# Kernel optimization log

Hardware: AMD Instinct MI355X
Metric: run time of the kernel (lower is better)

Reference implementation:

```python
import jax, jax.numpy as jnp
import numpy as np

N_FFT = 2048
HOP = 512
SR = 48000
T = 2_880_000  # 60 s stereo @ 48 kHz, multiple of HOP


def _hann(n):
    # torch.hann_window default (periodic=True)
    return (0.5 - 0.5 * jnp.cos(2.0 * jnp.pi * jnp.arange(n) / n)).astype(jnp.float32)


def _stft(x, win):
    # x: [C, T] -> [C, F, bins] complex64 (torch.stft center=True, reflect pad)
    pad = N_FFT // 2
    xp = jnp.pad(x, ((0, 0), (pad, pad)), mode='reflect')
    n_frames = 1 + (xp.shape[-1] - N_FFT) // HOP
    idx = jnp.arange(n_frames)[:, None] * HOP + jnp.arange(N_FFT)[None, :]
    frames = xp[:, idx] * win  # [C, F, N_FFT]
    return jnp.fft.rfft(frames, axis=-1)


def _istft(S, win, length):
    # S: [C, F, bins] -> [C, length]; overlap-add with window-square normalization
    frames = jnp.fft.irfft(S, n=N_FFT, axis=-1) * win  # [C, F, N_FFT]
    nF = frames.shape[1]
    total = (nF - 1) * HOP + N_FFT
    idx = jnp.arange(nF)[:, None] * HOP + jnp.arange(N_FFT)[None, :]
    ola = jnp.zeros((frames.shape[0], total), frames.dtype).at[:, idx].add(frames)
    wsum = jnp.zeros((total,), win.dtype).at[idx].add(jnp.broadcast_to(win ** 2, idx.shape))
    out = ola / jnp.where(wsum > 1e-11, wsum, 1.0)
    pad = N_FFT // 2
    return out[:, pad:pad + length]


def _eq_band(audio, freq, gain_db, q=1.0):
    win = _hann(N_FFT)
    S = _stft(audio, win)  # [C, F, bins]
    bins = S.shape[-1]
    freqs = jnp.linspace(0.0, 24000.0, bins)
    mask = jnp.exp(-((freqs - freq) / (freq / q)) ** 2)  # [bins]
    g_lin = 10.0 ** (gain_db / 20.0)
    S = S * (1.0 + (g_lin - 1.0) * mask)
    return _istft(S, win, audio.shape[-1])


def _compress(audio, threshold, ratio, attack, release, makeup_gain):
    aa = jnp.abs(audio) + 1e-8
    adb = 20.0 * jnp.log10(aa)
    gr = jnp.maximum(adb - threshold, 0.0) * (1.0 - 1.0 / ratio)  # [C, T]
    a_att = 1.0 - jnp.exp(-1.0 / (attack * SR))
    a_rel = 1.0 - jnp.exp(-1.0 / (release * SR))

    def step(prev, g):
        alpha = jnp.where(g > prev, a_att, a_rel)
        new = (1.0 - alpha) * prev + alpha * g
        return new, new

    init = jnp.zeros((audio.shape[0],), audio.dtype)
    _, gs = jax.lax.scan(step, init, gr[:, 1:].T)  # [T-1, C]
    gain_smooth = jnp.concatenate([init[:, None], gs.T], axis=1)  # [C, T]
    gain_lin = 10.0 ** ((-gain_smooth + makeup_gain) / 20.0)
    return jnp.sign(audio) * aa * gain_lin


def setup_inputs() -> dict:
    key = jax.random.key(0)
    audio = 0.1 * jax.random.normal(key, (2, T), dtype=jnp.float32)
    f32 = lambda v: jnp.float32(v)
    return {
        'audio': audio,
        'eq_low_gain': f32(3.0),
        'eq_low_mid_gain': f32(-2.0),
        'eq_high_mid_gain': f32(2.5),
        'eq_high_gain': f32(1.5),
        'comp_threshold': f32(-18.0),
        'comp_ratio': f32(4.0),
        'comp_attack': f32(0.01),
        'comp_release': f32(0.1),
        'comp_makeup_gain': f32(3.0),
        'saturation': f32(1.5),
    }


def reference(audio, eq_low_gain, eq_low_mid_gain, eq_high_mid_gain, eq_high_gain,
              comp_threshold, comp_ratio, comp_attack, comp_release,
              comp_makeup_gain, saturation):
    x = _eq_band(audio, 100.0, eq_low_gain)
    x = _eq_band(x, 500.0, eq_low_mid_gain)
    x = _eq_band(x, 3000.0, eq_high_mid_gain)
    x = _eq_band(x, 10000.0, eq_high_gain)
    x = _compress(x, comp_threshold, comp_ratio, comp_attack, comp_release, comp_makeup_gain)
    # saturation branch (original: python if on .item(); here jnp.where)
    return jnp.where(saturation > 1.0, jnp.tanh(x * saturation) / saturation, x)
```

## Files before the change

kernel.cpp:

```cpp
#include <hip/hip_runtime.h>
#include <math.h>

#define T_LEN   2880000
#define LASTFR  5625
#define NBLK_EQ 625
#define SEG     7680
#define NSEG    375
#define KREC    15
#define NREC    512
#define PROWS   528
#define RST     384
#define PL      (PROWS * RST)
#define SPL     (NREC * RST)

typedef float2 c2;
__device__ __forceinline__ c2 cadd(c2 a, c2 b){ return make_float2(a.x+b.x, a.y+b.y); }
__device__ __forceinline__ c2 csub(c2 a, c2 b){ return make_float2(a.x-b.x, a.y-b.y); }
__device__ __forceinline__ c2 cmul(c2 a, c2 b){ return make_float2(a.x*b.x - a.y*b.y, a.x*b.y + a.y*b.x); }
__device__ __forceinline__ c2 cmulj(c2 a, c2 b){ return make_float2(a.x*b.x + a.y*b.y, a.y*b.x - a.x*b.y); }

template<int SGN>
__device__ __forceinline__ void dft8(c2 v[8]) {
    const float r = 0.70710678118654752f;
    c2 t0 = cadd(v[0], v[4]), t1 = csub(v[0], v[4]);
    c2 t2 = cadd(v[2], v[6]), t3 = csub(v[2], v[6]);
    c2 u0 = cadd(v[1], v[5]), u1 = csub(v[1], v[5]);
    c2 u2 = cadd(v[3], v[7]), u3 = csub(v[3], v[7]);
    c2 t3r = (SGN < 0) ? make_float2(t3.y, -t3.x) : make_float2(-t3.y, t3.x);
    c2 u3r = (SGN < 0) ? make_float2(u3.y, -u3.x) : make_float2(-u3.y, u3.x);
    c2 E0 = cadd(t0, t2), E2 = csub(t0, t2);
    c2 E1 = cadd(t1, t3r), E3 = csub(t1, t3r);
    c2 O0 = cadd(u0, u2), O2 = csub(u0, u2);
    c2 O1 = cadd(u1, u3r), O3 = csub(u1, u3r);
    c2 O1w = (SGN < 0) ? make_float2(r*(O1.x+O1.y), r*(O1.y-O1.x))
                       : make_float2(r*(O1.x-O1.y), r*(O1.x+O1.y));
    c2 O2w = (SGN < 0) ? make_float2(O2.y, -O2.x) : make_float2(-O2.y, O2.x);
    c2 O3w = (SGN < 0) ? make_float2(r*(O3.y-O3.x), -r*(O3.x+O3.y))
                       : make_float2(-r*(O3.x+O3.y), r*(O3.x-O3.y));
    v[0] = cadd(E0, O0);  v[4] = csub(E0, O0);
    v[1] = cadd(E1, O1w); v[5] = csub(E1, O1w);
    v[2] = cadd(E2, O2w); v[6] = csub(E2, O2w);
    v[3] = cadd(E3, O3w); v[7] = csub(E3, O3w);
}

__device__ __forceinline__ c2 shx(c2 v, int m) {
    return make_float2(__shfl_xor(v.x, m), __shfl_xor(v.y, m));
}

__device__ __forceinline__ void emit_chunk(float* __restrict__ dst, const float* __restrict__ WN,
                                           int cchunk, int tid, c2 r0, c2 r1) {
    const bool edge = (cchunk <= 2) || (cchunk >= 5626);
    #pragma unroll
    for (int q = 0; q < 2; ++q) {
        c2 rr = (q == 0) ? r0 : r1;
        int m = cchunk * 512 + (q << 8) + tid;
        float inv = 0.66666666666667f;
        if (edge) {
            int tmn = (m >= 2048) ? (((m - 2048) >> 9) + 1) : 0;
            int tmx = min(LASTFR, m >> 9);
            float wsum = 0.0f;
            for (int tt = tmn; tt <= tmx; ++tt) {
                float w = WN[m - (tt << 9)];
                wsum += w * w;
            }
            inv = (wsum > 1e-11f) ? (1.0f / wsum) : 1.0f;
        }
        int o = m - 1024;
        dst[o]         = rr.x * inv;
        dst[T_LEN + o] = rr.y * inv;
    }
}

__global__ __launch_bounds__(256) void eq_band_kernel(
    const float* __restrict__ src, float* __restrict__ dst,
    const float* __restrict__ gain_db_p, const float f0)
{
    __shared__ c2 SA[2048];
    __shared__ c2 TWs1[2048];
    __shared__ c2 TWs2[256];
    __shared__ c2 TWs3[32];
    __shared__ float MKs[2048];
    __shared__ float WN[2048];

    const int tid = threadIdx.x;
    const int b   = blockIdx.x;

    const float gdb   = *gain_db_p;
    const float g_lin = exp2f(gdb * 0.16609640474436813f);
    const float gm1   = g_lin - 1.0f;

    const float st2048 = 6.283185307179586f / 2048.0f;
    for (int idx = tid; idx < 2048; idx += 256) {
        int m = idx >> 8, j = idx & 255;
        float ang = st2048 * (float)(j * m);
        TWs1[idx] = make_float2(cosf(ang), -sinf(ang));
        WN[idx] = 0.5f - 0.5f * cosf(st2048 * (float)idx);
        int tt = idx & 255;
        int bb = tt >> 2, jj = tt & 3;
        int qrev = ((jj & 1) << 1) | (jj >> 1);
        int k = (bb >> 3) + ((bb & 7) << 3) + (m << 6) + (qrev << 9);
        int kk = (k > 1024) ? (2048 - k) : k;
        float f = (float)kk * (24000.0f / 1024.0f);
        float d = (f - f0) / f0;
        MKs[idx] = (1.0f + gm1 * expf(-d * d)) * (1.0f / 2048.0f);
    }
    {
        int m = tid >> 5, j2 = tid & 31;
        float ang = (6.283185307179586f / 256.0f) * (float)(j2 * m);
        TWs2[tid] = make_float2(cosf(ang), -sinf(ang));
    }
    if (tid < 32) {
        int m = tid >> 2, j = tid & 3;
        float ang = (6.283185307179586f / 32.0f) * (float)(j * m);
        TWs3[tid] = make_float2(cosf(ang), -sinf(ang));
    }
    __syncthreads();

    const int t0   = max(0, 9 * b - 1);
    const int t1   = min(LASTFR, 9 * b + 10);
    const int cmin = 9 * b + 2;
    const int cmax = 9 * b + 10;

    c2 ring[8];
    #pragma unroll
    for (int q = 0; q < 8; ++q) ring[q] = make_float2(0.0f, 0.0f);

    for (int t = t0; t <= t1; ++t) {
        for (int j = tid; j < 2048; j += 256) {
            int ss = t * 512 + j - 1024;
            ss = (ss < 0) ? -ss : ss;
            ss = (ss >= T_LEN) ? (2 * T_LEN - 2 - ss) : ss;
            float w = WN[j];
            SA[j] = make_float2(src[ss] * w, src[T_LEN + ss] * w);
        }
        __syncthreads();

        c2 v[8];

        #pragma unroll
        for (int k = 0; k < 8; ++k) v[k] = SA[tid + (k << 8)];
        dft8<-1>(v);
        #pragma unroll
        for (int m = 1; m < 8; ++m) v[m] = cmul(v[m], TWs1[(m << 8) + tid]);
        #pragma unroll
        for (int m = 0; m < 8; ++m) SA[tid + (m << 8)] = v[m];
        __syncthreads();

        {
            int c = tid >> 5, j2 = tid & 31;
            int base = (c << 8) + j2;
            #pragma unroll
            for (int k = 0; k < 8; ++k) v[k] = SA[base + (k << 5)];
            dft8<-1>(v);
            #pragma unroll
            for (int m = 1; m < 8; ++m) v[m] = cmul(v[m], TWs2[(m << 5) + j2]);
            __syncthreads();
            #pragma unroll
            for (int m = 0; m < 8; ++m) SA[(c << 8) + (m << 5) + (j2 ^ (m << 2))] = v[m];
        }
        __syncthreads();

        {
            int bb = tid >> 2, j = tid & 3;
            int base = bb << 5, bx = (bb & 7) << 2;
            #pragma unroll
            for (int k = 0; k < 8; ++k) v[k] = SA[base + ((k << 2) ^ bx) + j];
            dft8<-1>(v);
            #pragma unroll
            for (int m = 1; m < 8; ++m) v[m] = cmul(v[m], TWs3[(m << 2) + j]);
            #pragma unroll
            for (int m = 0; m < 8; ++m) {
                c2 w = v[m];
                c2 p = shx(w, 2);
                c2 e  = (j & 2) ? csub(p, w) : cadd(w, p);
                c2 qq = shx(e, 1);
                c2 lo = (j & 1) ? csub(qq, e) : cadd(e, qq);
                c2 hi = (j & 1) ? make_float2(qq.x - e.y, qq.y + e.x)
                                : make_float2(e.x + qq.y, e.y - qq.x);
                w = (j & 2) ? hi : lo;
                float mk = MKs[(m << 8) + tid];
                w.x *= mk; w.y *= mk;
                c2 p2 = shx(w, 1);
                c2 e2 = (j & 1) ? csub(p2, w) : cadd(w, p2);
                c2 q2 = shx(e2, 2);
                c2 lo2 = (j & 1) ? make_float2(e2.x - q2.y, e2.y + q2.x)
                                 : cadd(e2, q2);
                c2 hi2 = (j & 1) ? make_float2(q2.x + e2.y, q2.y - e2.x)
                                 : csub(q2, e2);
                v[m] = (j & 2) ? hi2 : lo2;
            }
            #pragma unroll
            for (int m = 1; m < 8; ++m) v[m] = cmulj(v[m], TWs3[(m << 2) + j]);
            dft8<+1>(v);
            __syncthreads();
            #pragma unroll
            for (int k = 0; k < 8; ++k) SA[base + ((k << 2) ^ bx) + j] = v[k];
        }
        __syncthreads();

        {
            int c = tid >> 5, j2 = tid & 31;
            #pragma unroll
            for (int m = 0; m < 8; ++m) v[m] = SA[(c << 8) + (m << 5) + (j2 ^ (m << 2))];
            #pragma unroll
            for (int m = 1; m < 8; ++m) v[m] = cmulj(v[m], TWs2[(m << 5) + j2]);
            dft8<+1>(v);
            __syncthreads();
            #pragma unroll
            for (int k = 0; k < 8; ++k) SA[(c << 8) + (k << 5) + j2] = v[k];
        }
        __syncthreads();

        {
            #pragma unroll
            for (int m = 0; m < 8; ++m) v[m] = SA[tid + (m << 8)];
            #pragma unroll
            for (int m = 1; m < 8; ++m) v[m] = cmulj(v[m], TWs1[(m << 8) + tid]);
            dft8<+1>(v);
            #pragma unroll
            for (int k = 0; k < 8; ++k) {
                float w = WN[tid + (k << 8)];
                ring[k].x += v[k].x * w;
                ring[k].y += v[k].y * w;
            }
        }
        __syncthreads();

        if (t >= cmin) emit_chunk(dst, WN, t, tid, ring[0], ring[1]);
        #pragma unroll
        for (int q = 0; q < 6; ++q) ring[q] = ring[q + 2];
        ring[6] = make_float2(0.0f, 0.0f);
        ring[7] = make_float2(0.0f, 0.0f);
    }
    for (int c = t1 + 1; c <= cmax; ++c) {
        emit_chunk(dst, WN, c, tid, ring[0], ring[1]);
        #pragma unroll
        for (int q = 0; q < 6; ++q) ring[q] = ring[q + 2];
        ring[6] = make_float2(0.0f, 0.0f);
        ring[7] = make_float2(0.0f, 0.0f);
    }
}

__device__ __forceinline__ float gaval(float v, float thr, float coef) {
    float aa = fabsf(v) + 1e-8f;
    return fmaxf(6.020599913279624f * __log2f(aa) - thr, 0.0f) * coef;
}

__global__ __launch_bounds__(256) void rec15_kernel(
    const float* __restrict__ y, float4* __restrict__ rec,
    const float* __restrict__ thr_p, const float* __restrict__ ratio_p,
    const float* __restrict__ att_p, const float* __restrict__ rel_p)
{
    __shared__ float4 Lsub[32][9][4];
    const int r0 = blockIdx.x * 32;
    const int s0 = blockIdx.y * 64;
    const int c  = blockIdx.z;
    const int tid = threadIdx.x;

    float thr = *thr_p, ratio = *ratio_p;
    float A  = expf(-1.0f / ((*att_p) * 48000.0f));
    float Bc = expf(-1.0f / ((*rel_p) * 48000.0f));
    float ra = (1.0f - Bc) / (1.0f - A);
    float coef = (1.0f - 1.0f / ratio) * (1.0f - A);

    const int rr = tid & 31, cg = tid >> 5;
    const int orow = tid >> 3, oc8 = tid & 7;

    #pragma unroll 1
    for (int it = 0; it < 8; ++it) {
        int s = s0 + it * 8 + cg;
        if (s < NSEG) {
            int r = r0 + rr;
            int li = s * SEG + KREC * r;
            const float* yp = y + (long)c * T_LEN + li;
            float I[16];
            float a = gaval(yp[0], thr, coef);
            if (li == 0) a = 0.0f;
            I[0] = a; I[1] = ra * a;
            #pragma unroll
            for (int n = 1; n < KREC; ++n) {
                a = gaval(yp[n], thr, coef);
                float b = ra * a;
                I[n + 1] = fmaf(Bc, I[n], b);
                #pragma unroll
                for (int j = n; j >= 1; --j)
                    I[j] = fmaxf(fmaf(A, I[j], a), fmaf(Bc, I[j - 1], b));
                I[0] = fmaf(A, I[0], a);
            }
            Lsub[rr][cg][0] = make_float4(I[0],  I[1],  I[2],  I[3]);
            Lsub[rr][cg][1] = make_float4(I[4],  I[5],  I[6],  I[7]);
            Lsub[rr][cg][2] = make_float4(I[8],  I[9],  I[10], I[11]);
            Lsub[rr][cg][3] = make_float4(I[12], I[13], I[14], I[15]);
        }
        __syncthreads();
        int so = s0 + it * 8 + oc8;
        if (so < NSEG) {
            #pragma unroll
            for (int q = 0; q < 4; ++q)
                rec[(long)(c * 4 + q) * PL + (r0 + orow) * RST + 4 + so]
                    = Lsub[orow][oc8][q];
        }
        __syncthreads();
    }
}


struct Rec { float4 a, b, c, d; };

__device__ __forceinline__ void load8(Rec (&bb)[8],
    const float4* p0, const float4* p1, const float4* p2, const float4* p3, int r)
{
    #pragma unroll
    for (int k = 0; k < 8; ++k) {
        int o = (r + k) * RST;
        bb[k].a = p0[o]; bb[k].b = p1[o]; bb[k].c = p2[o]; bb[k].d = p3[o];
    }
}

template<bool STORE>
__device__ __forceinline__ void consume8(Rec (&bb)[8], float* sp, int r, float& p,
                                         const float (&S)[16])
{
    #pragma unroll
    for (int k = 0; k < 8; ++k) {
        Rec v = bb[k];
        float m0 = fmaxf(fmaf(S[0],  p, v.a.x), fmaf(S[1],  p, v.a.y));
        float m1 = fmaxf(fmaf(S[2],  p, v.a.z), fmaf(S[3],  p, v.a.w));
        float m2 = fmaxf(fmaf(S[4],  p, v.b.x), fmaf(S[5],  p, v.b.y));
        float m3 = fmaxf(fmaf(S[6],  p, v.b.z), fmaf(S[7],  p, v.b.w));
        float m4 = fmaxf(fmaf(S[8],  p, v.c.x), fmaf(S[9],  p, v.c.y));
        float m5 = fmaxf(fmaf(S[10], p, v.c.z), fmaf(S[11], p, v.c.w));
        float m6 = fmaxf(fmaf(S[12], p, v.d.x), fmaf(S[13], p, v.d.y));
        float m7 = fmaxf(fmaf(S[14], p, v.d.z), fmaf(S[15], p, v.d.w));
        m0 = fmaxf(m0, m1); m2 = fmaxf(m2, m3);
        m4 = fmaxf(m4, m5); m6 = fmaxf(m6, m7);
        m0 = fmaxf(m0, m2); m4 = fmaxf(m4, m6);
        p = fmaxf(m0, m4);
        if (STORE) sp[(r + k) * RST] = p;
    }
}

template<bool STORE>
__device__ void scan_pass(const float4* p0, const float4* p1, const float4* p2,
                          const float4* p3, float* sp, float& p, const float (&S)[16])
{
    Rec bA[8], bB[8];
    load8(bA, p0, p1, p2, p3, 0);
    __builtin_amdgcn_sched_barrier(0);
    int r = 0;
    #pragma unroll 1
    for (int gg = 0; gg < NREC / 16; ++gg) {
        load8(bB, p0, p1, p2, p3, r + 8);
        __builtin_amdgcn_sched_barrier(0);
        consume8<STORE>(bA, sp, r, p, S);
        __builtin_amdgcn_sched_barrier(0);
        load8(bA, p0, p1, p2, p3, r + 16);
        __builtin_amdgcn_sched_barrier(0);
        consume8<STORE>(bB, sp, r + 8, p, S);
        __builtin_amdgcn_sched_barrier(0);
        r += 16;
    }
}

template<int MODE>
__global__ __launch_bounds__(64, 1) void scan_iter_kernel(
    const float4* __restrict__ rec, float* __restrict__ gsP,
    const float* __restrict__ eIn, float* __restrict__ eOut,
    const float* __restrict__ att_p, const float* __restrict__ rel_p)
{
    int gid = blockIdx.x * 64 + threadIdx.x;
    int g2 = min(gid, 2 * NSEG - 1);
    int c = g2 / NSEG;
    int s = g2 - c * NSEG;

    float A  = expf(-1.0f / ((*att_p) * 48000.0f));
    float Bc = expf(-1.0f / ((*rel_p) * 48000.0f));
    float S[16];
    {
        float pa = 1.0f;
        #pragma unroll
        for (int j = 15; j >= 0; --j) { S[j] = pa; pa *= A; }
        float pb = 1.0f;
        #pragma unroll
        for (int j = 0; j < 16; ++j) { S[j] *= pb; pb *= Bc; }
    }

    float p = 0.0f;
    if (MODE != 0) p = (s == 0) ? 0.0f : eIn[c * NSEG + s - 1];

    const float4* p0 = rec + (long)(c * 4 + 0) * PL + 4 + s;
    const float4* p1 = rec + (long)(c * 4 + 1) * PL + 4 + s;
    const float4* p2 = rec + (long)(c * 4 + 2) * PL + 4 + s;
    const float4* p3 = rec + (long)(c * 4 + 3) * PL + 4 + s;

    if (MODE == 2) {
        float* sbase = gsP + (long)c * SPL + 4 + s;
        scan_pass<true>(p0, p1, p2, p3, sbase, p, S);
    } else {
        scan_pass<false>(p0, p1, p2, p3, nullptr, p, S);
        eOut[c * NSEG + s] = p;
    }
}

__global__ __launch_bounds__(256) void final_kernel(
    const float* __restrict__ y, const float* __restrict__ gsP, float* __restrict__ out,
    const float* __restrict__ thr_p, const float* __restrict__ ratio_p,
    const float* __restrict__ att_p, const float* __restrict__ rel_p,
    const float* __restrict__ mk_p, const float* __restrict__ sat_p)
{
    __shared__ float LP[64][34];
    const int r0 = blockIdx.x * 32;
    const int s0 = blockIdx.y * 64;
    const int c  = blockIdx.z;
    const int tid = threadIdx.x;

    float thr = *thr_p, ratio = *ratio_p, mk = *mk_p, sat = *sat_p;
    float A  = expf(-1.0f / ((*att_p) * 48000.0f));
    float Bc = expf(-1.0f / ((*rel_p) * 48000.0f));
    float ra = (1.0f - Bc) / (1.0f - A);
    float coef = (1.0f - 1.0f / ratio) * (1.0f - A);
    const float* gb = gsP + (long)c * SPL;

    for (int idx = tid; idx < 33 * 64; idx += 256) {
        int rr = idx >> 6, ss = idx & 63;
        int s = s0 + ss;
        float v = 0.0f;
        if (s < NSEG) {
            int row = r0 - 1 + rr;
            if (row >= 0)      v = gb[row * RST + 4 + s];
            else if (s > 0)    v = gb[(NREC - 1) * RST + 4 + s - 1];
        }
        LP[ss][rr] = v;
    }
    __syncthreads();

    #pragma unroll 1
    for (int it = 0; it < 8; ++it) {
        int idx = it * 256 + tid;
        int ss = idx >> 5, rr = idx & 31;
        int s = s0 + ss;
        if (s >= NSEG) continue;
        int r = r0 + rr;
        int li = s * SEG + KREC * r;
        const float* yp = y + (long)c * T_LEN + li;
        float* op = out + (long)c * T_LEN + li;
        float p = LP[ss][rr];
        #pragma unroll
        for (int q = 0; q < KREC; ++q) {
            float v = yp[q];
            float a = gaval(v, thr, coef);
            if (li + q == 0) a = 0.0f;
            p = fmaxf(fmaf(A, p, a), fmaf(Bc, p, ra * a));
            float aa = fabsf(v) + 1e-8f;
            float gl = exp2f((mk - p) * 0.16609640474436813f);
            float ro = aa * gl;
            ro = (v < 0.0f) ? -ro : ro;
            if (sat > 1.0f) ro = tanhf(ro * sat) / sat;
            op[q] = ro;
        }
    }
}

extern "C" void kernel_launch(void* const* d_in, const int* in_sizes, int n_in,
                              void* d_out, int out_size, void* d_ws, size_t ws_size,
                              hipStream_t stream)
{
    const float* audio = (const float*)d_in[0];
    const float* g1    = (const float*)d_in[1];
    const float* g2    = (const float*)d_in[2];
    const float* g3    = (const float*)d_in[3];
    const float* g4    = (const float*)d_in[4];
    const float* thr   = (const float*)d_in[5];
    const float* ratio = (const float*)d_in[6];
    const float* att   = (const float*)d_in[7];
    const float* rel   = (const float*)d_in[8];
    const float* mkup  = (const float*)d_in[9];
    const float* sat   = (const float*)d_in[10];

    float* out  = (float*)d_out;
    float* bufA = (float*)d_ws;
    float4* rec = (float4*)(bufA + 2 * T_LEN);
    float*  gsP = (float*)(rec + 8 * (long)PL);
    float*  eA  = gsP + 2 * (long)SPL;
    float*  eB  = eA + 2 * NSEG;

    eq_band_kernel<<<NBLK_EQ, 256, 0, stream>>>(audio, out,  g1, 100.0f);
    eq_band_kernel<<<NBLK_EQ, 256, 0, stream>>>(out,   bufA, g2, 500.0f);
    eq_band_kernel<<<NBLK_EQ, 256, 0, stream>>>(bufA,  out,  g3, 3000.0f);
    eq_band_kernel<<<NBLK_EQ, 256, 0, stream>>>(out,   bufA, g4, 10000.0f);

    dim3 tgrid(NREC / 32, (NSEG + 63) / 64, 2);
    rec15_kernel<<<tgrid, 256, 0, stream>>>(bufA, rec, thr, ratio, att, rel);

    scan_iter_kernel<0><<<12, 64, 0, stream>>>(rec, gsP, nullptr, eA, att, rel);
    scan_iter_kernel<1><<<12, 64, 0, stream>>>(rec, gsP, eA, eB, att, rel);
    scan_iter_kernel<1><<<12, 64, 0, stream>>>(rec, gsP, eB, eA, att, rel);
    scan_iter_kernel<1><<<12, 64, 0, stream>>>(rec, gsP, eA, eB, att, rel);
    scan_iter_kernel<2><<<12, 64, 0, stream>>>(rec, gsP, eB, nullptr, att, rel);

    final_kernel<<<tgrid, 256, 0, stream>>>(bufA, gsP, out,
                                            thr, ratio, att, rel, mkup, sat);
}
```

Before: 770.0 us.

## Warp-specialize scan kernel with producer waves staging records through LDS

The scan kernel now runs 256-thread blocks. Three producer waves load the next 8 rows of recurrence records into a double-buffered LDS tile while a fourth consumer wave runs the serial max-plus scan from the current tile. Before this, one wave both issued the global loads and did the dependent scan with software prefetch in registers. The goal is to hide global-memory latency behind the serial chain. In exchange, every round adds a block-wide barrier and an LDS round trip, and the launch still uses only 12 blocks.

```diff
diff --git a/kernel.cpp b/kernel.cpp
--- a/kernel.cpp
+++ b/kernel.cpp
@@ -305,73 +305,42 @@
 }
 
 
-struct Rec { float4 a, b, c, d; };
-
-__device__ __forceinline__ void load8(Rec (&bb)[8],
-    const float4* p0, const float4* p1, const float4* p2, const float4* p3, int r)
-{
+__device__ __forceinline__ void stage_round(
+    float4 (*LBs)[4][64], const float4* __restrict__ rec,
+    int wave, int lane, int colp, int c, int R0)
+{
+    float4 v[11];
     #pragma unroll
-    for (int k = 0; k < 8; ++k) {
-        int o = (r + k) * RST;
-        bb[k].a = p0[o]; bb[k].b = p1[o]; bb[k].c = p2[o]; bb[k].d = p3[o];
-    }
-}
-
-template<bool STORE>
-__device__ __forceinline__ void consume8(Rec (&bb)[8], float* sp, int r, float& p,
-                                         const float (&S)[16])
-{
+    for (int i = 0; i < 11; ++i) {
+        int w = wave + 3 * i;
+        if (w < 32) {
+            int q = w & 3, r = w >> 2;
+            v[i] = rec[(long)(c * 4 + q) * PL + (long)(R0 + r) * RST + colp];
+        }
+    }
     #pragma unroll
-    for (int k = 0; k < 8; ++k) {
-        Rec v = bb[k];
-        float m0 = fmaxf(fmaf(S[0],  p, v.a.x), fmaf(S[1],  p, v.a.y));
-        float m1 = fmaxf(fmaf(S[2],  p, v.a.z), fmaf(S[3],  p, v.a.w));
-        float m2 = fmaxf(fmaf(S[4],  p, v.b.x), fmaf(S[5],  p, v.b.y));
-        float m3 = fmaxf(fmaf(S[6],  p, v.b.z), fmaf(S[7],  p, v.b.w));
-        float m4 = fmaxf(fmaf(S[8],  p, v.c.x), fmaf(S[9],  p, v.c.y));
-        float m5 = fmaxf(fmaf(S[10], p, v.c.z), fmaf(S[11], p, v.c.w));
-        float m6 = fmaxf(fmaf(S[12], p, v.d.x), fmaf(S[13], p, v.d.y));
-        float m7 = fmaxf(fmaf(S[14], p, v.d.z), fmaf(S[15], p, v.d.w));
-        m0 = fmaxf(m0, m1); m2 = fmaxf(m2, m3);
-        m4 = fmaxf(m4, m5); m6 = fmaxf(m6, m7);
-        m0 = fmaxf(m0, m2); m4 = fmaxf(m4, m6);
-        p = fmaxf(m0, m4);
-        if (STORE) sp[(r + k) * RST] = p;
-    }
-}
-
-template<bool STORE>
-__device__ void scan_pass(const float4* p0, const float4* p1, const float4* p2,
-                          const float4* p3, float* sp, float& p, const float (&S)[16])
-{
-    Rec bA[8], bB[8];
-    load8(bA, p0, p1, p2, p3, 0);
-    __builtin_amdgcn_sched_barrier(0);
-    int r = 0;
-    #pragma unroll 1
-    for (int gg = 0; gg < NREC / 16; ++gg) {
-        load8(bB, p0, p1, p2, p3, r + 8);
-        __builtin_amdgcn_sched_barrier(0);
-        consume8<STORE>(bA, sp, r, p, S);
-        __builtin_amdgcn_sched_barrier(0);
-        load8(bA, p0, p1, p2, p3, r + 16);
-        __builtin_amdgcn_sched_barrier(0);
-        consume8<STORE>(bB, sp, r + 8, p, S);
-        __builtin_amdgcn_sched_barrier(0);
-        r += 16;
+    for (int i = 0; i < 11; ++i) {
+        int w = wave + 3 * i;
+        if (w < 32) {
+            int q = w & 3, r = w >> 2;
+            LBs[r][q][lane] = v[i];
+        }
     }
 }
 
 template<int MODE>
-__global__ __launch_bounds__(64, 1) void scan_iter_kernel(
+__global__ __launch_bounds__(256) void scan_iter_kernel(
     const float4* __restrict__ rec, float* __restrict__ gsP,
     const float* __restrict__ eIn, float* __restrict__ eOut,
     const float* __restrict__ att_p, const float* __restrict__ rel_p)
 {
-    int gid = blockIdx.x * 64 + threadIdx.x;
-    int g2 = min(gid, 2 * NSEG - 1);
-    int c = g2 / NSEG;
-    int s = g2 - c * NSEG;
+    __shared__ float4 LB[2][8][4][64];
+    const int tid  = threadIdx.x;
+    const int wave = tid >> 6, lane = tid & 63;
+    const int c    = blockIdx.x / 6;
+    const int c0   = (blockIdx.x % 6) * 64;
+    const int s    = min(c0 + lane, NSEG - 1);
+    const int colp = 4 + s;
 
     float A  = expf(-1.0f / ((*att_p) * 48000.0f));
     float Bc = expf(-1.0f / ((*rel_p) * 48000.0f));
@@ -387,19 +356,41 @@
 
     float p = 0.0f;
     if (MODE != 0) p = (s == 0) ? 0.0f : eIn[c * NSEG + s - 1];
-
-    const float4* p0 = rec + (long)(c * 4 + 0) * PL + 4 + s;
-    const float4* p1 = rec + (long)(c * 4 + 1) * PL + 4 + s;
-    const float4* p2 = rec + (long)(c * 4 + 2) * PL + 4 + s;
-    const float4* p3 = rec + (long)(c * 4 + 3) * PL + 4 + s;
-
-    if (MODE == 2) {
-        float* sbase = gsP + (long)c * SPL + 4 + s;
-        scan_pass<true>(p0, p1, p2, p3, sbase, p, S);
-    } else {
-        scan_pass<false>(p0, p1, p2, p3, nullptr, p, S);
-        eOut[c * NSEG + s] = p;
-    }
+    float* sp = gsP + (long)c * SPL + 4 + s;
+
+    if (wave < 3) stage_round(LB[0], rec, wave, lane, colp, c, 0);
+    __syncthreads();
+
+    #pragma unroll 1
+    for (int t = 0; t < NREC / 8; ++t) {
+        if (wave < 3) {
+            if (t < 63) stage_round(LB[(t + 1) & 1], rec, wave, lane, colp, c,
+                                    (t + 1) * 8);
+        } else {
+            #pragma unroll
+            for (int k = 0; k < 8; ++k) {
+                float4 va = LB[t & 1][k][0][lane];
+                float4 vb = LB[t & 1][k][1][lane];
+                float4 vc = LB[t & 1][k][2][lane];
+                float4 vd = LB[t & 1][k][3][lane];
+                float m0 = fmaxf(fmaf(S[0],  p, va.x), fmaf(S[1],  p, va.y));
+                float m1 = fmaxf(fmaf(S[2],  p, va.z), fmaf(S[3],  p, va.w));
+                float m2 = fmaxf(fmaf(S[4],  p, vb.x), fmaf(S[5],  p, vb.y));
+                float m3 = fmaxf(fmaf(S[6],  p, vb.z), fmaf(S[7],  p, vb.w));
+                float m4 = fmaxf(fmaf(S[8],  p, vc.x), fmaf(S[9],  p, vc.y));
+                float m5 = fmaxf(fmaf(S[10], p, vc.z), fmaf(S[11], p, vc.w));
+                float m6 = fmaxf(fmaf(S[12], p, vd.x), fmaf(S[13], p, vd.y));
+                float m7 = fmaxf(fmaf(S[14], p, vd.z), fmaf(S[15], p, vd.w));
+                m0 = fmaxf(m0, m1); m2 = fmaxf(m2, m3);
+                m4 = fmaxf(m4, m5); m6 = fmaxf(m6, m7);
+                m0 = fmaxf(m0, m2); m4 = fmaxf(m4, m6);
+                p = fmaxf(m0, m4);
+                if (MODE == 2) sp[(t * 8 + k) * RST] = p;
+            }
+        }
+        __syncthreads();
+    }
+    if (wave == 3 && MODE != 2) eOut[c * NSEG + s] = p;
 }
 
 __global__ __launch_bounds__(256) void final_kernel(
@@ -492,11 +483,11 @@
     dim3 tgrid(NREC / 32, (NSEG + 63) / 64, 2);
     rec15_kernel<<<tgrid, 256, 0, stream>>>(bufA, rec, thr, ratio, att, rel);
 
-    scan_iter_kernel<0><<<12, 64, 0, stream>>>(rec, gsP, nullptr, eA, att, rel);
-    scan_iter_kernel<1><<<12, 64, 0, stream>>>(rec, gsP, eA, eB, att, rel);
-    scan_iter_kernel<1><<<12, 64, 0, stream>>>(rec, gsP, eB, eA, att, rel);
-    scan_iter_kernel<1><<<12, 64, 0, stream>>>(rec, gsP, eA, eB, att, rel);
-    scan_iter_kernel<2><<<12, 64, 0, stream>>>(rec, gsP, eB, nullptr, att, rel);
+    scan_iter_kernel<0><<<12, 256, 0, stream>>>(rec, gsP, nullptr, eA, att, rel);
+    scan_iter_kernel<1><<<12, 256, 0, stream>>>(rec, gsP, eA, eB, att, rel);
+    scan_iter_kernel<1><<<12, 256, 0, stream>>>(rec, gsP, eB, eA, att, rel);
+    scan_iter_kernel<1><<<12, 256, 0, stream>>>(rec, gsP, eA, eB, att, rel);
+    scan_iter_kernel<2><<<12, 256, 0, stream>>>(rec, gsP, eB, nullptr, att, rel);
 
     final_kernel<<<tgrid, 256, 0, stream>>>(bufA, gsP, out,
                                             thr, ratio, att, rel, mkup, sat);
```

New measurement: 832.5 us. 1.08x slower.
